# Performance work log

Measured on AMD Instinct MI355X. Metric: run time of the kernel, lower is better.

The kernel has to match this reference:

```python
import jax, jax.numpy as jnp
import numpy as np

B, N, DH, DG, HID, K_STEPS, CURV = 256, 2048, 128, 256, 256, 2, 1.0
SC = CURV ** 0.5
SCALE = 1.0 / (DH ** 0.5)
LN_EPS = 1e-5


def _artanh(x):
    return jnp.arctanh(jnp.clip(x, -1.0 + 1e-5, 1.0 - 1e-5))


def logmap0(x, sc=SC):
    n = jnp.maximum(jnp.linalg.norm(x, axis=-1, keepdims=True), 1e-7)
    return x * (_artanh(sc * n) / (sc * n))


def expmap0(v, sc=SC):
    n = jnp.maximum(jnp.linalg.norm(v, axis=-1, keepdims=True), 1e-7)
    return v * (jnp.tanh(sc * n) / (sc * n))


def setup_inputs() -> dict:
    key = jax.random.key(0)
    ks = jax.random.split(key, 16)

    def lin(k, out_d, in_d):
        return (jax.random.normal(k, (out_d, in_d), jnp.float32) * (in_d ** -0.5))

    demo_hyp = expmap0(0.1 * jax.random.normal(ks[0], (B, N, DH), jnp.float32))
    rho_g = jax.random.normal(ks[1], (B, DG), jnp.float32)
    return {
        "demo_hyp": demo_hyp,
        "rho_g": rho_g,
        "seed_g_w": lin(ks[2], DH, DG),
        "seed_g_b": jnp.zeros((DH,), jnp.float32),
        "seed_d_w": lin(ks[3], DH, DH),
        "pool_wq_w": lin(ks[4], DH, DH),
        "pool_wk_w": lin(ks[5], DH, DH),
        "pool_wv_w": lin(ks[6], DH, DH),
        "q_u_w": lin(ks[7], DH, DH),
        "q_g_w": lin(ks[8], DH, DG),
        "q_g_b": jnp.zeros((DH,), jnp.float32),
        "kv_w": lin(ks[9], DH, DH),
        "mlp_w1": lin(ks[10], HID, DH),
        "mlp_b1": jnp.zeros((HID,), jnp.float32),
        "mlp_w2": lin(ks[11], DH, HID),
        "mlp_b2": jnp.zeros((DH,), jnp.float32),
        "ln_g": jnp.ones((DH,), jnp.float32),
        "ln_b": jnp.zeros((DH,), jnp.float32),
    }


def reference(demo_hyp, rho_g, seed_g_w, seed_g_b, seed_d_w,
              pool_wq_w, pool_wk_w, pool_wv_w, q_u_w, q_g_w, q_g_b,
              kv_w, mlp_w1, mlp_b1, mlp_w2, mlp_b2, ln_g, ln_b):
    demo_tan = logmap0(demo_hyp)                       # (B,N,Dh)

    # seed: attention-pool demos with rho_g query
    q_seed = rho_g @ seed_g_w.T + seed_g_b             # (B,Dh)
    qk = q_seed @ pool_wq_w.T                          # (B,Dh)
    Kp = demo_tan @ pool_wk_w.T                        # (B,N,Dh)
    a = jax.nn.softmax(jnp.einsum('bd,bnd->bn', qk, Kp) * SCALE, axis=-1)
    Vp = demo_tan @ pool_wv_w.T
    pooled = jnp.einsum('bn,bnd->bd', a, Vp)           # (B,Dh)
    u = expmap0(q_seed + pooled @ seed_d_w.T)

    for _ in range(K_STEPS):
        u_tan = logmap0(u)
        mu = jnp.mean(u_tan, axis=-1, keepdims=True)
        var = jnp.var(u_tan, axis=-1, keepdims=True)
        u_tan = (u_tan - mu) * jax.lax.rsqrt(var + LN_EPS) * ln_g + ln_b
        q = u_tan @ q_u_w.T + rho_g @ q_g_w.T + q_g_b
        Kmat = demo_tan @ kv_w.T                       # keys == values
        att = jax.nn.softmax(jnp.einsum('bd,bnd->bn', q, Kmat) * SCALE, axis=-1)
        delta = jnp.einsum('bn,bnd->bd', att, Kmat)
        upd = jax.nn.gelu(delta @ mlp_w1.T + mlp_b1, approximate=False) @ mlp_w2.T + mlp_b2
        u = expmap0(u_tan + upd)
    return u
```

## Files before the change

### kernel.cpp

```cpp
#include <hip/hip_runtime.h>
#include <cstddef>
#include <cstdint>

#define B 256
#define N 2048
#define DH 128
#define DG 256
#define HID 256
#define SPLITS 8
#define CHUNK (N / SPLITS)
#define ROWS_PER_ITER 32
#define KITER (CHUNK / ROWS_PER_ITER)
#define SCALE 0.08838834764831845f
#define LN_EPS 1e-5f
#define TAN_NORM_MAX 6.2f


__device__ __forceinline__ float artanh_clip(float a) {
  a = fminf(a, 1.0f - 1e-5f);
  return 0.5f * __logf((1.0f + a) / (1.0f - a));
}

__device__ __forceinline__ float logmap_scale(float n2) {
  float nc = fmaxf(sqrtf(n2), 1e-7f);
  return artanh_clip(nc) / nc;
}

__device__ __forceinline__ float row16_sum(float x) {
  x += __int_as_float(__builtin_amdgcn_update_dpp(0, __float_as_int(x), 0x128, 0xF, 0xF, true));
  x += __int_as_float(__builtin_amdgcn_update_dpp(0, __float_as_int(x), 0x124, 0xF, 0xF, true));
  x += __int_as_float(__builtin_amdgcn_update_dpp(0, __float_as_int(x), 0x122, 0xF, 0xF, true));
  x += __int_as_float(__builtin_amdgcn_update_dpp(0, __float_as_int(x), 0x121, 0xF, 0xF, true));
  return x;
}

__device__ __forceinline__ float dotN(const float* __restrict__ wrow,
                                      const float* __restrict__ x, int n4) {
  const float4* a = (const float4*)wrow;
  const float4* bx = (const float4*)x;
  float s = 0.f;
  for (int j = 0; j < n4; ++j) {
    float4 u = a[j], v = bx[j];
    s += u.x * v.x + u.y * v.y + u.z * v.z + u.w * v.w;
  }
  return s;
}

__device__ __forceinline__ float blockSum128(float v, float* s_red) {
#pragma unroll
  for (int msk = 1; msk < 64; msk <<= 1) v += __shfl_xor(v, msk);
  if ((threadIdx.x & 63) == 0) s_red[threadIdx.x >> 6] = v;
  __syncthreads();
  float r = s_red[0] + s_red[1];
  __syncthreads();
  return r;
}

__device__ __forceinline__ float combine_partials(const float* __restrict__ partials,
                                                  int b, int tid) {
  const float* pb = partials + (size_t)b * SPLITS * (DH + 2);
  float L = 0.f, a = 0.f;
#pragma unroll
  for (int s = 0; s < SPLITS; ++s) {
    L += pb[s * (DH + 2) + DH];
    a += pb[s * (DH + 2) + tid];
  }
  return a / L;
}


__global__ void setup_pool_query(const float* __restrict__ rho,
                                 const float* __restrict__ seed_g_w,
                                 const float* __restrict__ seed_g_b,
                                 const float* __restrict__ pool_wq_w,
                                 const float* __restrict__ pool_wk_w,
                                 float* __restrict__ q_seed,
                                 float* __restrict__ qvec,
                                 float* __restrict__ mb) {
  const int b = blockIdx.x, tid = threadIdx.x;
  __shared__ __align__(16) float s_rho[DG];
  __shared__ __align__(16) float s_qs[DH];
  __shared__ __align__(16) float s_qk[DH];
  __shared__ float s_red[2];
  s_rho[tid] = rho[b * DG + tid];
  s_rho[tid + DH] = rho[b * DG + tid + DH];
  __syncthreads();
  float qs = seed_g_b[tid] + dotN(seed_g_w + (size_t)tid * DG, s_rho, DG / 4);
  q_seed[b * DH + tid] = qs;
  s_qs[tid] = qs;
  __syncthreads();
  float qk = dotN(pool_wq_w + (size_t)tid * DH, s_qs, DH / 4);
  s_qk[tid] = qk;
  __syncthreads();
  float qp = 0.f;
  for (int i = 0; i < DH; ++i) qp += pool_wk_w[i * DH + tid] * s_qk[i];
  qvec[b * DH + tid] = qp;
  float qn2 = blockSum128(qp * qp, s_red);
  if (tid == 0) mb[b] = SCALE * TAN_NORM_MAX * sqrtf(qn2);
}


template <int LOADTS>
__global__ __launch_bounds__(256, 6) void attn_pass(const float* __restrict__ demo,
                                                    const float* __restrict__ qvec,
                                                    const float* __restrict__ mb,
                                                    float* __restrict__ partials,
                                                    float* __restrict__ ts_buf) {
  const int blk = blockIdx.x;
  const int b = blk >> 3;
  const int s = blk & 7;
  const int tid = threadIdx.x;
  const int w = tid >> 6;
  const int lane = tid & 63;
  const int g = lane >> 4;
  const int il = lane & 15;

  const float4 qv0 = *(const float4*)(qvec + b * DH + il * 4);
  const float4 qv1 = *(const float4*)(qvec + b * DH + 64 + il * 4);
  const float Mb = mb[b];

  const size_t row0 = (size_t)b * N + (size_t)s * CHUNK + (size_t)(w * 8);
  const float* p = demo + (row0 + g) * DH + il * 4;
  const size_t rts = row0 + g;

  float lsum = 0.f;
  float4 accL = make_float4(0.f, 0.f, 0.f, 0.f);
  float4 accH = make_float4(0.f, 0.f, 0.f, 0.f);

  float4 xa1 = *(const float4*)(p);
  float4 xa2 = *(const float4*)(p + 64);
  float4 xb1 = *(const float4*)(p + 4 * DH);
  float4 xb2 = *(const float4*)(p + 4 * DH + 64);
  float tsA = 0.f, tsB = 0.f;
  if (LOADTS) { tsA = ts_buf[rts]; tsB = ts_buf[rts + 4]; }

  for (int k = 0; k < KITER; ++k) {
    float4 ca1 = xa1, ca2 = xa2, cb1 = xb1, cb2 = xb2;
    float tA = tsA, tB = tsB;
    if (k + 1 < KITER) {
      const float* pn = p + (size_t)(k + 1) * ROWS_PER_ITER * DH;
      xa1 = *(const float4*)(pn);
      xa2 = *(const float4*)(pn + 64);
      xb1 = *(const float4*)(pn + 4 * DH);
      xb2 = *(const float4*)(pn + 4 * DH + 64);
      if (LOADTS) {
        tsA = ts_buf[rts + (size_t)(k + 1) * ROWS_PER_ITER];
        tsB = ts_buf[rts + (size_t)(k + 1) * ROWS_PER_ITER + 4];
      }
    }
    {
      float dd = qv0.x * ca1.x + qv0.y * ca1.y + qv0.z * ca1.z + qv0.w * ca1.w +
                 qv1.x * ca2.x + qv1.y * ca2.y + qv1.z * ca2.z + qv1.w * ca2.w;
      dd = row16_sum(dd);
      float tsv;
      if (LOADTS) {
        tsv = tA;
      } else {
        float n2 = ca1.x * ca1.x + ca1.y * ca1.y + ca1.z * ca1.z + ca1.w * ca1.w +
                   ca2.x * ca2.x + ca2.y * ca2.y + ca2.z * ca2.z + ca2.w * ca2.w;
        n2 = row16_sum(n2);
        tsv = logmap_scale(n2);
        if (il == 0) ts_buf[rts + (size_t)k * ROWS_PER_ITER] = tsv;
      }
      float pw = __expf(dd * tsv * SCALE - Mb);
      lsum += pw;
      float c = pw * tsv;
      accL.x += c * ca1.x; accL.y += c * ca1.y; accL.z += c * ca1.z; accL.w += c * ca1.w;
      accH.x += c * ca2.x; accH.y += c * ca2.y; accH.z += c * ca2.z; accH.w += c * ca2.w;
    }
    {
      float dd = qv0.x * cb1.x + qv0.y * cb1.y + qv0.z * cb1.z + qv0.w * cb1.w +
                 qv1.x * cb2.x + qv1.y * cb2.y + qv1.z * cb2.z + qv1.w * cb2.w;
      dd = row16_sum(dd);
      float tsv;
      if (LOADTS) {
        tsv = tB;
      } else {
        float n2 = cb1.x * cb1.x + cb1.y * cb1.y + cb1.z * cb1.z + cb1.w * cb1.w +
                   cb2.x * cb2.x + cb2.y * cb2.y + cb2.z * cb2.z + cb2.w * cb2.w;
        n2 = row16_sum(n2);
        tsv = logmap_scale(n2);
        if (il == 0) ts_buf[rts + (size_t)k * ROWS_PER_ITER + 4] = tsv;
      }
      float pw = __expf(dd * tsv * SCALE - Mb);
      lsum += pw;
      float c = pw * tsv;
      accL.x += c * cb1.x; accL.y += c * cb1.y; accL.z += c * cb1.z; accL.w += c * cb1.w;
      accH.x += c * cb2.x; accH.y += c * cb2.y; accH.z += c * cb2.z; accH.w += c * cb2.w;
    }
  }

  __shared__ __align__(16) float s_acc[16][DH];
  __shared__ float s_l[16];
  const int slot = (w << 2) | g;
  *(float4*)&s_acc[slot][il * 4] = accL;
  *(float4*)&s_acc[slot][64 + il * 4] = accH;
  if (il == 0) s_l[slot] = lsum;
  __syncthreads();
  if (tid < DH) {
    float a = 0.f;
#pragma unroll
    for (int j = 0; j < 16; ++j) a += s_acc[j][tid];
    float* pp = partials + (size_t)blk * (DH + 2);
    pp[tid] = a;
    if (tid == 0) {
      float L = 0.f;
#pragma unroll
      for (int j = 0; j < 16; ++j) L += s_l[j];
      pp[DH] = L;
    }
  }
}


__global__ void trans_pool(const float* __restrict__ partials,
                           const float* __restrict__ q_seed,
                           const float* __restrict__ rho,
                           const float* __restrict__ pool_wv_w,
                           const float* __restrict__ seed_d_w,
                           const float* __restrict__ q_u_w,
                           const float* __restrict__ q_g_w,
                           const float* __restrict__ q_g_b,
                           const float* __restrict__ kv_w,
                           const float* __restrict__ ln_g,
                           const float* __restrict__ ln_b,
                           float* __restrict__ u_tan_out,
                           float* __restrict__ qvec_out,
                           float* __restrict__ mb) {
  const int b = blockIdx.x, tid = threadIdx.x;
  __shared__ __align__(16) float s_a[DH];
  __shared__ __align__(16) float s_b[DH];
  __shared__ __align__(16) float s_rho[DG];
  __shared__ float s_red[2];

  float w0 = combine_partials(partials, b, tid);
  s_a[tid] = w0;
  s_rho[tid] = rho[b * DG + tid];
  s_rho[tid + DH] = rho[b * DG + tid + DH];
  __syncthreads();
  float pooled = dotN(pool_wv_w + (size_t)tid * DH, s_a, DH / 4);
  s_b[tid] = pooled;
  __syncthreads();
  float v = q_seed[b * DH + tid] + dotN(seed_d_w + (size_t)tid * DH, s_b, DH / 4);
  float n2 = blockSum128(v * v, s_red);
  float nc = fmaxf(sqrtf(n2), 1e-7f);
  float u = v * (tanhf(nc) / nc);
  float nu2 = blockSum128(u * u, s_red);
  float nuc = fmaxf(sqrtf(nu2), 1e-7f);
  float ut = u * (artanh_clip(nuc) / nuc);
  float mu = blockSum128(ut, s_red) * (1.0f / DH);
  float d = ut - mu;
  float var = blockSum128(d * d, s_red) * (1.0f / DH);
  float y = d * rsqrtf(var + LN_EPS) * ln_g[tid] + ln_b[tid];
  u_tan_out[b * DH + tid] = y;
  s_a[tid] = y;
  __syncthreads();
  float q = q_g_b[tid] + dotN(q_u_w + (size_t)tid * DH, s_a, DH / 4) +
            dotN(q_g_w + (size_t)tid * DG, s_rho, DG / 4);
  s_b[tid] = q;
  __syncthreads();
  float qp = 0.f;
  for (int i = 0; i < DH; ++i) qp += kv_w[i * DH + tid] * s_b[i];
  qvec_out[b * DH + tid] = qp;
  float qn2 = blockSum128(qp * qp, s_red);
  if (tid == 0) mb[b] = SCALE * TAN_NORM_MAX * sqrtf(qn2);
}


__global__ void trans_iter(const float* __restrict__ partials,
                           const float* __restrict__ u_tan_in,
                           const float* __restrict__ rho,
                           const float* __restrict__ kv_w,
                           const float* __restrict__ mlp_w1,
                           const float* __restrict__ mlp_b1,
                           const float* __restrict__ mlp_w2,
                           const float* __restrict__ mlp_b2,
                           const float* __restrict__ q_u_w,
                           const float* __restrict__ q_g_w,
                           const float* __restrict__ q_g_b,
                           const float* __restrict__ ln_g,
                           const float* __restrict__ ln_b,
                           float* __restrict__ u_tan_out,
                           float* __restrict__ qvec_out,
                           float* __restrict__ mb,
                           float* __restrict__ out, int is_final) {
  const int b = blockIdx.x, tid = threadIdx.x;
  __shared__ __align__(16) float s_a[DH];
  __shared__ __align__(16) float s_b[DH];
  __shared__ __align__(16) float s_h[HID];
  __shared__ __align__(16) float s_rho[DG];
  __shared__ float s_red[2];

  float wv = combine_partials(partials, b, tid);
  s_a[tid] = wv;
  s_rho[tid] = rho[b * DG + tid];
  s_rho[tid + DH] = rho[b * DG + tid + DH];
  __syncthreads();
  float delta = dotN(kv_w + (size_t)tid * DH, s_a, DH / 4);
  s_b[tid] = delta;
  __syncthreads();
  float h0 = mlp_b1[tid] + dotN(mlp_w1 + (size_t)tid * DH, s_b, DH / 4);
  float h1 = mlp_b1[tid + DH] + dotN(mlp_w1 + (size_t)(tid + DH) * DH, s_b, DH / 4);
  s_h[tid] = 0.5f * h0 * (1.0f + erff(h0 * 0.70710678118654752f));
  s_h[tid + DH] = 0.5f * h1 * (1.0f + erff(h1 * 0.70710678118654752f));
  __syncthreads();
  float upd = mlp_b2[tid] + dotN(mlp_w2 + (size_t)tid * HID, s_h, HID / 4);
  float v = u_tan_in[b * DH + tid] + upd;
  float n2 = blockSum128(v * v, s_red);
  float nc = fmaxf(sqrtf(n2), 1e-7f);
  float u = v * (tanhf(nc) / nc);
  if (is_final) {
    out[b * DH + tid] = u;
    return;
  }
  float nu2 = blockSum128(u * u, s_red);
  float nuc = fmaxf(sqrtf(nu2), 1e-7f);
  float ut = u * (artanh_clip(nuc) / nuc);
  float mu = blockSum128(ut, s_red) * (1.0f / DH);
  float d = ut - mu;
  float var = blockSum128(d * d, s_red) * (1.0f / DH);
  float y = d * rsqrtf(var + LN_EPS) * ln_g[tid] + ln_b[tid];
  u_tan_out[b * DH + tid] = y;
  s_a[tid] = y;
  __syncthreads();
  float q = q_g_b[tid] + dotN(q_u_w + (size_t)tid * DH, s_a, DH / 4) +
            dotN(q_g_w + (size_t)tid * DG, s_rho, DG / 4);
  s_b[tid] = q;
  __syncthreads();
  float qp = 0.f;
  for (int i = 0; i < DH; ++i) qp += kv_w[i * DH + tid] * s_b[i];
  qvec_out[b * DH + tid] = qp;
  float qn2 = blockSum128(qp * qp, s_red);
  if (tid == 0) mb[b] = SCALE * TAN_NORM_MAX * sqrtf(qn2);
}


extern "C" void kernel_launch(void* const* d_in, const int* in_sizes, int n_in,
                              void* d_out, int out_size, void* d_ws, size_t ws_size,
                              hipStream_t stream) {
  const float* demo      = (const float*)d_in[0];
  const float* rho       = (const float*)d_in[1];
  const float* seed_g_w  = (const float*)d_in[2];
  const float* seed_g_b  = (const float*)d_in[3];
  const float* seed_d_w  = (const float*)d_in[4];
  const float* pool_wq_w = (const float*)d_in[5];
  const float* pool_wk_w = (const float*)d_in[6];
  const float* pool_wv_w = (const float*)d_in[7];
  const float* q_u_w     = (const float*)d_in[8];
  const float* q_g_w     = (const float*)d_in[9];
  const float* q_g_b     = (const float*)d_in[10];
  const float* kv_w      = (const float*)d_in[11];
  const float* mlp_w1    = (const float*)d_in[12];
  const float* mlp_b1    = (const float*)d_in[13];
  const float* mlp_w2    = (const float*)d_in[14];
  const float* mlp_b2    = (const float*)d_in[15];
  const float* ln_g      = (const float*)d_in[16];
  const float* ln_b      = (const float*)d_in[17];
  float* out = (float*)d_out;

  float* ws = (float*)d_ws;
  float* qvec  = ws;
  float* qseed = ws + B * DH;
  float* utanA = ws + 2 * B * DH;
  float* utanB = ws + 3 * B * DH;
  float* mb    = ws + 4 * B * DH;
  float* parts = ws + 4 * B * DH + B;
  float* tsbuf = parts + B * SPLITS * (DH + 2);

  setup_pool_query<<<B, DH, 0, stream>>>(rho, seed_g_w, seed_g_b, pool_wq_w,
                                         pool_wk_w, qseed, qvec, mb);
  attn_pass<0><<<B * SPLITS, 256, 0, stream>>>(demo, qvec, mb, parts, tsbuf);
  trans_pool<<<B, DH, 0, stream>>>(parts, qseed, rho, pool_wv_w, seed_d_w,
                                   q_u_w, q_g_w, q_g_b, kv_w, ln_g, ln_b,
                                   utanA, qvec, mb);
  attn_pass<1><<<B * SPLITS, 256, 0, stream>>>(demo, qvec, mb, parts, tsbuf);
  trans_iter<<<B, DH, 0, stream>>>(parts, utanA, rho, kv_w, mlp_w1, mlp_b1,
                                   mlp_w2, mlp_b2, q_u_w, q_g_w, q_g_b, ln_g,
                                   ln_b, utanB, qvec, mb, out, 0);
  attn_pass<1><<<B * SPLITS, 256, 0, stream>>>(demo, qvec, mb, parts, tsbuf);
  trans_iter<<<B, DH, 0, stream>>>(parts, utanB, rho, kv_w, mlp_w1, mlp_b1,
                                   mlp_w2, mlp_b2, q_u_w, q_g_w, q_g_b, ln_g,
                                   ln_b, utanB, qvec, mb, out, 1);
}
```

Baseline: 602.8 us.

## Fuse all refinement stages into one persistent per-batch kernel

Replaces the seven-kernel pipeline (setup, three attention passes with split partials, and transform kernels) with a single kernel where one 512-thread block handles a whole batch row. It removes launch gaps, partial-sum buffers and global round trips for query vectors, and recomputes the logmap scale each pass instead of storing it. The cost is fewer, larger blocks (256 blocks total), which lowers the parallelism available for streaming demo data and serialises the small matvec phases between passes.

```diff
diff --git a/kernel.cpp b/kernel.cpp
--- a/kernel.cpp
+++ b/kernel.cpp
@@ -7,10 +7,10 @@
 #define DH 128
 #define DG 256
 #define HID 256
-#define SPLITS 8
-#define CHUNK (N / SPLITS)
-#define ROWS_PER_ITER 32
-#define KITER (CHUNK / ROWS_PER_ITER)
+#define WAVES 8
+#define TPB (WAVES * 64)
+#define RPI (WAVES * 8)
+#define KIT (N / RPI)
 #define SCALE 0.08838834764831845f
 #define LN_EPS 1e-5f
 #define TAN_NORM_MAX 6.2f
@@ -34,304 +34,246 @@
   return x;
 }
 
-__device__ __forceinline__ float dotN(const float* __restrict__ wrow,
-                                      const float* __restrict__ x, int n4) {
+__device__ __forceinline__ float wave_allsum(float v) {
+#pragma unroll
+  for (int m = 1; m < 64; m <<= 1) v += __shfl_xor(v, m);
+  return v;
+}
+
+__device__ __forceinline__ float dot128(const float* __restrict__ wrow,
+                                        const float* __restrict__ x) {
   const float4* a = (const float4*)wrow;
-  const float4* bx = (const float4*)x;
+  const float4* v = (const float4*)x;
   float s = 0.f;
-  for (int j = 0; j < n4; ++j) {
-    float4 u = a[j], v = bx[j];
-    s += u.x * v.x + u.y * v.y + u.z * v.z + u.w * v.w;
+#pragma unroll
+  for (int j = 0; j < 32; ++j) {
+    float4 u = a[j], b = v[j];
+    s += u.x * b.x + u.y * b.y + u.z * b.z + u.w * b.w;
   }
   return s;
 }
 
-__device__ __forceinline__ float blockSum128(float v, float* s_red) {
+__device__ __forceinline__ float dot256(const float* __restrict__ wrow,
+                                        const float* __restrict__ x) {
+  const float4* a = (const float4*)wrow;
+  const float4* v = (const float4*)x;
+  float s = 0.f;
 #pragma unroll
-  for (int msk = 1; msk < 64; msk <<= 1) v += __shfl_xor(v, msk);
-  if ((threadIdx.x & 63) == 0) s_red[threadIdx.x >> 6] = v;
-  __syncthreads();
-  float r = s_red[0] + s_red[1];
-  __syncthreads();
-  return r;
-}
-
-__device__ __forceinline__ float combine_partials(const float* __restrict__ partials,
-                                                  int b, int tid) {
-  const float* pb = partials + (size_t)b * SPLITS * (DH + 2);
-  float L = 0.f, a = 0.f;
-#pragma unroll
-  for (int s = 0; s < SPLITS; ++s) {
-    L += pb[s * (DH + 2) + DH];
-    a += pb[s * (DH + 2) + tid];
-  }
-  return a / L;
-}
-
-
-__global__ void setup_pool_query(const float* __restrict__ rho,
-                                 const float* __restrict__ seed_g_w,
-                                 const float* __restrict__ seed_g_b,
-                                 const float* __restrict__ pool_wq_w,
-                                 const float* __restrict__ pool_wk_w,
-                                 float* __restrict__ q_seed,
-                                 float* __restrict__ qvec,
-                                 float* __restrict__ mb) {
-  const int b = blockIdx.x, tid = threadIdx.x;
-  __shared__ __align__(16) float s_rho[DG];
-  __shared__ __align__(16) float s_qs[DH];
-  __shared__ __align__(16) float s_qk[DH];
-  __shared__ float s_red[2];
-  s_rho[tid] = rho[b * DG + tid];
-  s_rho[tid + DH] = rho[b * DG + tid + DH];
-  __syncthreads();
-  float qs = seed_g_b[tid] + dotN(seed_g_w + (size_t)tid * DG, s_rho, DG / 4);
-  q_seed[b * DH + tid] = qs;
-  s_qs[tid] = qs;
-  __syncthreads();
-  float qk = dotN(pool_wq_w + (size_t)tid * DH, s_qs, DH / 4);
-  s_qk[tid] = qk;
-  __syncthreads();
-  float qp = 0.f;
-  for (int i = 0; i < DH; ++i) qp += pool_wk_w[i * DH + tid] * s_qk[i];
-  qvec[b * DH + tid] = qp;
-  float qn2 = blockSum128(qp * qp, s_red);
-  if (tid == 0) mb[b] = SCALE * TAN_NORM_MAX * sqrtf(qn2);
-}
-
-
-template <int LOADTS>
-__global__ __launch_bounds__(256, 6) void attn_pass(const float* __restrict__ demo,
-                                                    const float* __restrict__ qvec,
-                                                    const float* __restrict__ mb,
-                                                    float* __restrict__ partials,
-                                                    float* __restrict__ ts_buf) {
-  const int blk = blockIdx.x;
-  const int b = blk >> 3;
-  const int s = blk & 7;
+  for (int j = 0; j < 64; ++j) {
+    float4 u = a[j], b = v[j];
+    s += u.x * b.x + u.y * b.y + u.z * b.z + u.w * b.w;
+  }
+  return s;
+}
+
+
+__global__ __launch_bounds__(TPB, 2) void fused_refiner(
+    const float* __restrict__ demo, const float* __restrict__ rho,
+    const float* __restrict__ seed_g_w, const float* __restrict__ seed_g_b,
+    const float* __restrict__ seed_d_w, const float* __restrict__ pool_wq_w,
+    const float* __restrict__ pool_wk_w, const float* __restrict__ pool_wv_w,
+    const float* __restrict__ q_u_w, const float* __restrict__ q_g_w,
+    const float* __restrict__ q_g_b, const float* __restrict__ kv_w,
+    const float* __restrict__ mlp_w1, const float* __restrict__ mlp_b1,
+    const float* __restrict__ mlp_w2, const float* __restrict__ mlp_b2,
+    const float* __restrict__ ln_g, const float* __restrict__ ln_b,
+    float* __restrict__ out) {
+  const int b = blockIdx.x;
   const int tid = threadIdx.x;
   const int w = tid >> 6;
   const int lane = tid & 63;
   const int g = lane >> 4;
   const int il = lane & 15;
 
-  const float4 qv0 = *(const float4*)(qvec + b * DH + il * 4);
-  const float4 qv1 = *(const float4*)(qvec + b * DH + 64 + il * 4);
-  const float Mb = mb[b];
-
-  const size_t row0 = (size_t)b * N + (size_t)s * CHUNK + (size_t)(w * 8);
-  const float* p = demo + (row0 + g) * DH + il * 4;
-  const size_t rts = row0 + g;
-
-  float lsum = 0.f;
-  float4 accL = make_float4(0.f, 0.f, 0.f, 0.f);
-  float4 accH = make_float4(0.f, 0.f, 0.f, 0.f);
-
-  float4 xa1 = *(const float4*)(p);
-  float4 xa2 = *(const float4*)(p + 64);
-  float4 xb1 = *(const float4*)(p + 4 * DH);
-  float4 xb2 = *(const float4*)(p + 4 * DH + 64);
-  float tsA = 0.f, tsB = 0.f;
-  if (LOADTS) { tsA = ts_buf[rts]; tsB = ts_buf[rts + 4]; }
-
-  for (int k = 0; k < KITER; ++k) {
-    float4 ca1 = xa1, ca2 = xa2, cb1 = xb1, cb2 = xb2;
-    float tA = tsA, tB = tsB;
-    if (k + 1 < KITER) {
-      const float* pn = p + (size_t)(k + 1) * ROWS_PER_ITER * DH;
-      xa1 = *(const float4*)(pn);
-      xa2 = *(const float4*)(pn + 64);
-      xb1 = *(const float4*)(pn + 4 * DH);
-      xb2 = *(const float4*)(pn + 4 * DH + 64);
-      if (LOADTS) {
-        tsA = ts_buf[rts + (size_t)(k + 1) * ROWS_PER_ITER];
-        tsB = ts_buf[rts + (size_t)(k + 1) * ROWS_PER_ITER + 4];
-      }
-    }
-    {
-      float dd = qv0.x * ca1.x + qv0.y * ca1.y + qv0.z * ca1.z + qv0.w * ca1.w +
-                 qv1.x * ca2.x + qv1.y * ca2.y + qv1.z * ca2.z + qv1.w * ca2.w;
-      dd = row16_sum(dd);
-      float tsv;
-      if (LOADTS) {
-        tsv = tA;
-      } else {
+  __shared__ __align__(16) float s_rho[DG];
+  __shared__ __align__(16) float s_x[DH];
+  __shared__ __align__(16) float s_y[DH];
+  __shared__ __align__(16) float s_h[HID];
+  __shared__ __align__(16) float s_ut[DH];
+  __shared__ __align__(16) float s_qseed[DH];
+  __shared__ __align__(16) float s_qvec[DH];
+  __shared__ __align__(16) float s_fold[WAVES][DH];
+  __shared__ float s_l[WAVES];
+  __shared__ float s_red[WAVES];
+  __shared__ float s_Mb;
+
+  auto bsumAll = [&](float v) -> float {
+    v = wave_allsum(v);
+    if (lane == 0) s_red[w] = v;
+    __syncthreads();
+    float r = s_red[0] + s_red[1] + s_red[2] + s_red[3] +
+              s_red[4] + s_red[5] + s_red[6] + s_red[7];
+    __syncthreads();
+    return r;
+  };
+
+  auto ln_query = [&](float v) {
+    float n2 = bsumAll(tid < DH ? v * v : 0.f);
+    float u = 0.f, ut = 0.f;
+    if (tid < DH) {
+      float nc = fmaxf(sqrtf(n2), 1e-7f);
+      u = v * (tanhf(nc) / nc);
+    }
+    float nu2 = bsumAll(tid < DH ? u * u : 0.f);
+    if (tid < DH) {
+      float nuc = fmaxf(sqrtf(nu2), 1e-7f);
+      ut = u * (artanh_clip(nuc) / nuc);
+    }
+    float mu = bsumAll(tid < DH ? ut : 0.f) * (1.0f / DH);
+    float d = ut - mu;
+    float var = bsumAll(tid < DH ? d * d : 0.f) * (1.0f / DH);
+    if (tid < DH) {
+      float y = d * rsqrtf(var + LN_EPS) * ln_g[tid] + ln_b[tid];
+      s_ut[tid] = y;
+      s_x[tid] = y;
+    }
+    __syncthreads();
+    if (tid < DH) {
+      s_y[tid] = q_g_b[tid] + dot128(q_u_w + (size_t)tid * DH, s_x) +
+                 dot256(q_g_w + (size_t)tid * DG, s_rho);
+    }
+    __syncthreads();
+    float qp = 0.f;
+    if (tid < DH) {
+#pragma unroll 8
+      for (int i = 0; i < DH; ++i) qp += kv_w[i * DH + tid] * s_y[i];
+      s_qvec[tid] = qp;
+    }
+    float qn2 = bsumAll(tid < DH ? qp * qp : 0.f);
+    if (tid == 0) s_Mb = SCALE * TAN_NORM_MAX * sqrtf(qn2);
+    __syncthreads();
+  };
+
+  if (tid < DG) s_rho[tid] = rho[(size_t)b * DG + tid];
+  __syncthreads();
+  if (tid < DH) {
+    float qs = seed_g_b[tid] + dot256(seed_g_w + (size_t)tid * DG, s_rho);
+    s_qseed[tid] = qs;
+    s_x[tid] = qs;
+  }
+  __syncthreads();
+  if (tid < DH) s_y[tid] = dot128(pool_wq_w + (size_t)tid * DH, s_x);
+  __syncthreads();
+  float qp0 = 0.f;
+  if (tid < DH) {
+#pragma unroll 8
+    for (int i = 0; i < DH; ++i) qp0 += pool_wk_w[i * DH + tid] * s_y[i];
+    s_qvec[tid] = qp0;
+  }
+  float qn2 = bsumAll(tid < DH ? qp0 * qp0 : 0.f);
+  if (tid == 0) s_Mb = SCALE * TAN_NORM_MAX * sqrtf(qn2);
+  __syncthreads();
+
+  const float* demo_b = demo + (size_t)b * N * DH;
+
+  for (int pass = 0; pass < 3; ++pass) {
+    const float4 qv0 = *(const float4*)&s_qvec[il * 4];
+    const float4 qv1 = *(const float4*)&s_qvec[64 + il * 4];
+    const float Mb = s_Mb;
+    const float* p = demo_b + (size_t)(w * 8 + g) * DH + il * 4;
+
+    float lsum = 0.f;
+    float4 accL = make_float4(0.f, 0.f, 0.f, 0.f);
+    float4 accH = make_float4(0.f, 0.f, 0.f, 0.f);
+
+    float4 xa1 = *(const float4*)(p);
+    float4 xa2 = *(const float4*)(p + 64);
+    float4 xb1 = *(const float4*)(p + 4 * DH);
+    float4 xb2 = *(const float4*)(p + 4 * DH + 64);
+
+    for (int k = 0; k < KIT; ++k) {
+      float4 ca1 = xa1, ca2 = xa2, cb1 = xb1, cb2 = xb2;
+      if (k + 1 < KIT) {
+        const float* pn = p + (size_t)(k + 1) * RPI * DH;
+        xa1 = *(const float4*)(pn);
+        xa2 = *(const float4*)(pn + 64);
+        xb1 = *(const float4*)(pn + 4 * DH);
+        xb2 = *(const float4*)(pn + 4 * DH + 64);
+      }
+      {
+        float dd = qv0.x * ca1.x + qv0.y * ca1.y + qv0.z * ca1.z + qv0.w * ca1.w +
+                   qv1.x * ca2.x + qv1.y * ca2.y + qv1.z * ca2.z + qv1.w * ca2.w;
         float n2 = ca1.x * ca1.x + ca1.y * ca1.y + ca1.z * ca1.z + ca1.w * ca1.w +
                    ca2.x * ca2.x + ca2.y * ca2.y + ca2.z * ca2.z + ca2.w * ca2.w;
+        dd = row16_sum(dd);
         n2 = row16_sum(n2);
-        tsv = logmap_scale(n2);
-        if (il == 0) ts_buf[rts + (size_t)k * ROWS_PER_ITER] = tsv;
-      }
-      float pw = __expf(dd * tsv * SCALE - Mb);
-      lsum += pw;
-      float c = pw * tsv;
-      accL.x += c * ca1.x; accL.y += c * ca1.y; accL.z += c * ca1.z; accL.w += c * ca1.w;
-      accH.x += c * ca2.x; accH.y += c * ca2.y; accH.z += c * ca2.z; accH.w += c * ca2.w;
-    }
-    {
-      float dd = qv0.x * cb1.x + qv0.y * cb1.y + qv0.z * cb1.z + qv0.w * cb1.w +
-                 qv1.x * cb2.x + qv1.y * cb2.y + qv1.z * cb2.z + qv1.w * cb2.w;
-      dd = row16_sum(dd);
-      float tsv;
-      if (LOADTS) {
-        tsv = tB;
-      } else {
+        float tsv = logmap_scale(n2);
+        float pw = __expf(dd * tsv * SCALE - Mb);
+        lsum += pw;
+        float c = pw * tsv;
+        accL.x += c * ca1.x; accL.y += c * ca1.y; accL.z += c * ca1.z; accL.w += c * ca1.w;
+        accH.x += c * ca2.x; accH.y += c * ca2.y; accH.z += c * ca2.z; accH.w += c * ca2.w;
+      }
+      {
+        float dd = qv0.x * cb1.x + qv0.y * cb1.y + qv0.z * cb1.z + qv0.w * cb1.w +
+                   qv1.x * cb2.x + qv1.y * cb2.y + qv1.z * cb2.z + qv1.w * cb2.w;
         float n2 = cb1.x * cb1.x + cb1.y * cb1.y + cb1.z * cb1.z + cb1.w * cb1.w +
                    cb2.x * cb2.x + cb2.y * cb2.y + cb2.z * cb2.z + cb2.w * cb2.w;
+        dd = row16_sum(dd);
         n2 = row16_sum(n2);
-        tsv = logmap_scale(n2);
-        if (il == 0) ts_buf[rts + (size_t)k * ROWS_PER_ITER + 4] = tsv;
-      }
-      float pw = __expf(dd * tsv * SCALE - Mb);
-      lsum += pw;
-      float c = pw * tsv;
-      accL.x += c * cb1.x; accL.y += c * cb1.y; accL.z += c * cb1.z; accL.w += c * cb1.w;
-      accH.x += c * cb2.x; accH.y += c * cb2.y; accH.z += c * cb2.z; accH.w += c * cb2.w;
-    }
-  }
-
-  __shared__ __align__(16) float s_acc[16][DH];
-  __shared__ float s_l[16];
-  const int slot = (w << 2) | g;
-  *(float4*)&s_acc[slot][il * 4] = accL;
-  *(float4*)&s_acc[slot][64 + il * 4] = accH;
-  if (il == 0) s_l[slot] = lsum;
-  __syncthreads();
-  if (tid < DH) {
-    float a = 0.f;
+        float tsv = logmap_scale(n2);
+        float pw = __expf(dd * tsv * SCALE - Mb);
+        lsum += pw;
+        float c = pw * tsv;
+        accL.x += c * cb1.x; accL.y += c * cb1.y; accL.z += c * cb1.z; accL.w += c * cb1.w;
+        accH.x += c * cb2.x; accH.y += c * cb2.y; accH.z += c * cb2.z; accH.w += c * cb2.w;
+      }
+    }
+
+    accL.x += __shfl_xor(accL.x, 16); accL.x += __shfl_xor(accL.x, 32);
+    accL.y += __shfl_xor(accL.y, 16); accL.y += __shfl_xor(accL.y, 32);
+    accL.z += __shfl_xor(accL.z, 16); accL.z += __shfl_xor(accL.z, 32);
+    accL.w += __shfl_xor(accL.w, 16); accL.w += __shfl_xor(accL.w, 32);
+    accH.x += __shfl_xor(accH.x, 16); accH.x += __shfl_xor(accH.x, 32);
+    accH.y += __shfl_xor(accH.y, 16); accH.y += __shfl_xor(accH.y, 32);
+    accH.z += __shfl_xor(accH.z, 16); accH.z += __shfl_xor(accH.z, 32);
+    accH.w += __shfl_xor(accH.w, 16); accH.w += __shfl_xor(accH.w, 32);
+    lsum += __shfl_xor(lsum, 16); lsum += __shfl_xor(lsum, 32);
+    if (g == 0) {
+      *(float4*)&s_fold[w][il * 4] = accL;
+      *(float4*)&s_fold[w][64 + il * 4] = accH;
+      if (il == 0) s_l[w] = lsum;
+    }
+    __syncthreads();
+
+    if (tid < DH) {
+      float a = 0.f;
 #pragma unroll
-    for (int j = 0; j < 16; ++j) a += s_acc[j][tid];
-    float* pp = partials + (size_t)blk * (DH + 2);
-    pp[tid] = a;
-    if (tid == 0) {
-      float L = 0.f;
-#pragma unroll
-      for (int j = 0; j < 16; ++j) L += s_l[j];
-      pp[DH] = L;
-    }
-  }
-}
-
-
-__global__ void trans_pool(const float* __restrict__ partials,
-                           const float* __restrict__ q_seed,
-                           const float* __restrict__ rho,
-                           const float* __restrict__ pool_wv_w,
-                           const float* __restrict__ seed_d_w,
-                           const float* __restrict__ q_u_w,
-                           const float* __restrict__ q_g_w,
-                           const float* __restrict__ q_g_b,
-                           const float* __restrict__ kv_w,
-                           const float* __restrict__ ln_g,
-                           const float* __restrict__ ln_b,
-                           float* __restrict__ u_tan_out,
-                           float* __restrict__ qvec_out,
-                           float* __restrict__ mb) {
-  const int b = blockIdx.x, tid = threadIdx.x;
-  __shared__ __align__(16) float s_a[DH];
-  __shared__ __align__(16) float s_b[DH];
-  __shared__ __align__(16) float s_rho[DG];
-  __shared__ float s_red[2];
-
-  float w0 = combine_partials(partials, b, tid);
-  s_a[tid] = w0;
-  s_rho[tid] = rho[b * DG + tid];
-  s_rho[tid + DH] = rho[b * DG + tid + DH];
-  __syncthreads();
-  float pooled = dotN(pool_wv_w + (size_t)tid * DH, s_a, DH / 4);
-  s_b[tid] = pooled;
-  __syncthreads();
-  float v = q_seed[b * DH + tid] + dotN(seed_d_w + (size_t)tid * DH, s_b, DH / 4);
-  float n2 = blockSum128(v * v, s_red);
-  float nc = fmaxf(sqrtf(n2), 1e-7f);
-  float u = v * (tanhf(nc) / nc);
-  float nu2 = blockSum128(u * u, s_red);
-  float nuc = fmaxf(sqrtf(nu2), 1e-7f);
-  float ut = u * (artanh_clip(nuc) / nuc);
-  float mu = blockSum128(ut, s_red) * (1.0f / DH);
-  float d = ut - mu;
-  float var = blockSum128(d * d, s_red) * (1.0f / DH);
-  float y = d * rsqrtf(var + LN_EPS) * ln_g[tid] + ln_b[tid];
-  u_tan_out[b * DH + tid] = y;
-  s_a[tid] = y;
-  __syncthreads();
-  float q = q_g_b[tid] + dotN(q_u_w + (size_t)tid * DH, s_a, DH / 4) +
-            dotN(q_g_w + (size_t)tid * DG, s_rho, DG / 4);
-  s_b[tid] = q;
-  __syncthreads();
-  float qp = 0.f;
-  for (int i = 0; i < DH; ++i) qp += kv_w[i * DH + tid] * s_b[i];
-  qvec_out[b * DH + tid] = qp;
-  float qn2 = blockSum128(qp * qp, s_red);
-  if (tid == 0) mb[b] = SCALE * TAN_NORM_MAX * sqrtf(qn2);
-}
-
-
-__global__ void trans_iter(const float* __restrict__ partials,
-                           const float* __restrict__ u_tan_in,
-                           const float* __restrict__ rho,
-                           const float* __restrict__ kv_w,
-                           const float* __restrict__ mlp_w1,
-                           const float* __restrict__ mlp_b1,
-                           const float* __restrict__ mlp_w2,
-                           const float* __restrict__ mlp_b2,
-                           const float* __restrict__ q_u_w,
-                           const float* __restrict__ q_g_w,
-                           const float* __restrict__ q_g_b,
-                           const float* __restrict__ ln_g,
-                           const float* __restrict__ ln_b,
-                           float* __restrict__ u_tan_out,
-                           float* __restrict__ qvec_out,
-                           float* __restrict__ mb,
-                           float* __restrict__ out, int is_final) {
-  const int b = blockIdx.x, tid = threadIdx.x;
-  __shared__ __align__(16) float s_a[DH];
-  __shared__ __align__(16) float s_b[DH];
-  __shared__ __align__(16) float s_h[HID];
-  __shared__ __align__(16) float s_rho[DG];
-  __shared__ float s_red[2];
-
-  float wv = combine_partials(partials, b, tid);
-  s_a[tid] = wv;
-  s_rho[tid] = rho[b * DG + tid];
-  s_rho[tid + DH] = rho[b * DG + tid + DH];
-  __syncthreads();
-  float delta = dotN(kv_w + (size_t)tid * DH, s_a, DH / 4);
-  s_b[tid] = delta;
-  __syncthreads();
-  float h0 = mlp_b1[tid] + dotN(mlp_w1 + (size_t)tid * DH, s_b, DH / 4);
-  float h1 = mlp_b1[tid + DH] + dotN(mlp_w1 + (size_t)(tid + DH) * DH, s_b, DH / 4);
-  s_h[tid] = 0.5f * h0 * (1.0f + erff(h0 * 0.70710678118654752f));
-  s_h[tid + DH] = 0.5f * h1 * (1.0f + erff(h1 * 0.70710678118654752f));
-  __syncthreads();
-  float upd = mlp_b2[tid] + dotN(mlp_w2 + (size_t)tid * HID, s_h, HID / 4);
-  float v = u_tan_in[b * DH + tid] + upd;
-  float n2 = blockSum128(v * v, s_red);
-  float nc = fmaxf(sqrtf(n2), 1e-7f);
-  float u = v * (tanhf(nc) / nc);
-  if (is_final) {
-    out[b * DH + tid] = u;
-    return;
-  }
-  float nu2 = blockSum128(u * u, s_red);
-  float nuc = fmaxf(sqrtf(nu2), 1e-7f);
-  float ut = u * (artanh_clip(nuc) / nuc);
-  float mu = blockSum128(ut, s_red) * (1.0f / DH);
-  float d = ut - mu;
-  float var = blockSum128(d * d, s_red) * (1.0f / DH);
-  float y = d * rsqrtf(var + LN_EPS) * ln_g[tid] + ln_b[tid];
-  u_tan_out[b * DH + tid] = y;
-  s_a[tid] = y;
-  __syncthreads();
-  float q = q_g_b[tid] + dotN(q_u_w + (size_t)tid * DH, s_a, DH / 4) +
-            dotN(q_g_w + (size_t)tid * DG, s_rho, DG / 4);
-  s_b[tid] = q;
-  __syncthreads();
-  float qp = 0.f;
-  for (int i = 0; i < DH; ++i) qp += kv_w[i * DH + tid] * s_b[i];
-  qvec_out[b * DH + tid] = qp;
-  float qn2 = blockSum128(qp * qp, s_red);
-  if (tid == 0) mb[b] = SCALE * TAN_NORM_MAX * sqrtf(qn2);
+      for (int j = 0; j < WAVES; ++j) a += s_fold[j][tid];
+      float L = s_l[0] + s_l[1] + s_l[2] + s_l[3] +
+                s_l[4] + s_l[5] + s_l[6] + s_l[7];
+      s_x[tid] = a / L;
+    }
+    __syncthreads();
+
+    if (pass == 0) {
+      if (tid < DH) s_y[tid] = dot128(pool_wv_w + (size_t)tid * DH, s_x);
+      __syncthreads();
+      float v = 0.f;
+      if (tid < DH) v = s_qseed[tid] + dot128(seed_d_w + (size_t)tid * DH, s_y);
+      ln_query(v);
+    } else {
+      if (tid < DH) s_y[tid] = dot128(kv_w + (size_t)tid * DH, s_x);
+      __syncthreads();
+      if (tid < HID) {
+        float h = mlp_b1[tid] + dot128(mlp_w1 + (size_t)tid * DH, s_y);
+        s_h[tid] = 0.5f * h * (1.0f + erff(h * 0.70710678118654752f));
+      }
+      __syncthreads();
+      float v = 0.f;
+      if (tid < DH)
+        v = s_ut[tid] + mlp_b2[tid] + dot256(mlp_w2 + (size_t)tid * HID, s_h);
+      if (pass == 2) {
+        float n2 = bsumAll(tid < DH ? v * v : 0.f);
+        if (tid < DH) {
+          float nc = fmaxf(sqrtf(n2), 1e-7f);
+          out[(size_t)b * DH + tid] = v * (tanhf(nc) / nc);
+        }
+      } else {
+        ln_query(v);
+      }
+    }
+  }
 }
 
 
@@ -357,28 +299,10 @@
   const float* ln_g      = (const float*)d_in[16];
   const float* ln_b      = (const float*)d_in[17];
   float* out = (float*)d_out;
-
-  float* ws = (float*)d_ws;
-  float* qvec  = ws;
-  float* qseed = ws + B * DH;
-  float* utanA = ws + 2 * B * DH;
-  float* utanB = ws + 3 * B * DH;
-  float* mb    = ws + 4 * B * DH;
-  float* parts = ws + 4 * B * DH + B;
-  float* tsbuf = parts + B * SPLITS * (DH + 2);
-
-  setup_pool_query<<<B, DH, 0, stream>>>(rho, seed_g_w, seed_g_b, pool_wq_w,
-                                         pool_wk_w, qseed, qvec, mb);
-  attn_pass<0><<<B * SPLITS, 256, 0, stream>>>(demo, qvec, mb, parts, tsbuf);
-  trans_pool<<<B, DH, 0, stream>>>(parts, qseed, rho, pool_wv_w, seed_d_w,
-                                   q_u_w, q_g_w, q_g_b, kv_w, ln_g, ln_b,
-                                   utanA, qvec, mb);
-  attn_pass<1><<<B * SPLITS, 256, 0, stream>>>(demo, qvec, mb, parts, tsbuf);
-  trans_iter<<<B, DH, 0, stream>>>(parts, utanA, rho, kv_w, mlp_w1, mlp_b1,
-                                   mlp_w2, mlp_b2, q_u_w, q_g_w, q_g_b, ln_g,
-                                   ln_b, utanB, qvec, mb, out, 0);
-  attn_pass<1><<<B * SPLITS, 256, 0, stream>>>(demo, qvec, mb, parts, tsbuf);
-  trans_iter<<<B, DH, 0, stream>>>(parts, utanB, rho, kv_w, mlp_w1, mlp_b1,
-                                   mlp_w2, mlp_b2, q_u_w, q_g_w, q_g_b, ln_g,
-                                   ln_b, utanB, qvec, mb, out, 1);
-}
+  (void)d_ws; (void)ws_size; (void)in_sizes; (void)n_in; (void)out_size;
+
+  fused_refiner<<<B, TPB, 0, stream>>>(demo, rho, seed_g_w, seed_g_b, seed_d_w,
+                                       pool_wq_w, pool_wk_w, pool_wv_w, q_u_w,
+                                       q_g_w, q_g_b, kv_w, mlp_w1, mlp_b1,
+                                       mlp_w2, mlp_b2, ln_g, ln_b, out);
+}
```

New measurement: 516.8 us. 1.17x faster.
